# Kernel optimization log

Measured on AMD Instinct MI355X. Metric: run time of the kernel, lower is better.

## Reference

```python
import jax, jax.numpy as jnp
import numpy as np

INF = 10000000000.0
D_KEY = 1024


def setup_inputs() -> dict:
    key = jax.random.key(0)
    k1, k2, k3 = jax.random.split(key, 3)
    B, S, D = 8, 2048, D_KEY
    return {
        "query": jax.random.normal(k1, (B, S, D), dtype=jnp.float32),
        "key": jax.random.normal(k2, (B, S, D), dtype=jnp.float32),
        "value": jax.random.normal(k3, (B, S, D), dtype=jnp.float32),
    }


def reference(query, key, value):
    # dot_products: [B, S, S]
    scale = jnp.asarray(np.sqrt(D_KEY), dtype=query.dtype)
    dots = jnp.einsum("bqd,bkd->bqk", query, key)
    S = key.shape[1]
    # causal mask: subtract INF on strictly-upper-triangular entries
    # (original subtracts mask BEFORE dividing by scale)
    tri = jnp.triu(jnp.ones((S, S), dtype=dots.dtype), k=1) * INF
    dots = dots - tri[None, :, :]
    attn = jax.nn.softmax(dots / scale, axis=-1)
    return jnp.einsum("bqk,bkd->bqd", attn, value)
```

## Files before the change

kernel.cpp:

```cpp
#include <hip/hip_runtime.h>

#define BB 8
#define SS 2048
#define DD 1024

typedef float f32x4 __attribute__((ext_vector_type(4)));
typedef short s16x8 __attribute__((ext_vector_type(8)));
typedef short s16x4 __attribute__((ext_vector_type(4)));

__device__ __forceinline__ short f2bf(float f) {
  unsigned u = __float_as_uint(f);
  u += 0x7FFFu + ((u >> 16) & 1u);
  return (short)(u >> 16);
}

__global__ __launch_bounds__(256)
void cvt_bf16(const float* __restrict__ s0, const float* __restrict__ s1,
              short* __restrict__ d0, short* __restrict__ d1) {
  const float* s = (blockIdx.y == 0) ? s0 : s1;
  short*       d = (blockIdx.y == 0) ? d0 : d1;
  size_t i = ((size_t)blockIdx.x * 256 + threadIdx.x) * 4;
  float4 v = *(const float4*)(s + i);
  s16x4 h = { f2bf(v.x), f2bf(v.y), f2bf(v.z), f2bf(v.w) };
  *(s16x4*)(d + i) = h;
}

__global__ __launch_bounds__(256)
void cvt_vT(const float* __restrict__ V, short* __restrict__ Vt) {
  __shared__ float tile[64][65];
  const int b  = blockIdx.z;
  const int k0 = blockIdx.x * 64;
  const int d0 = blockIdx.y * 64;

  const float* src = V + ((size_t)b * SS + k0) * DD + d0;
  {
    int row = threadIdx.x >> 4;
    int col = (threadIdx.x & 15) * 4;
    #pragma unroll
    for (int i = 0; i < 4; ++i) {
      float4 v = *(const float4*)(src + (size_t)(row + i * 16) * DD + col);
      tile[row + i * 16][col + 0] = v.x;
      tile[row + i * 16][col + 1] = v.y;
      tile[row + i * 16][col + 2] = v.z;
      tile[row + i * 16][col + 3] = v.w;
    }
  }
  __syncthreads();
  {
    int d  = threadIdx.x & 63;
    int kc = (threadIdx.x >> 6) * 16;
    short* dst = Vt + ((size_t)b * DD + d0 + d) * SS + k0 + kc;
    s16x8 h0, h1;
    #pragma unroll
    for (int j = 0; j < 8; ++j) h0[j] = f2bf(tile[kc + j][d]);
    #pragma unroll
    for (int j = 0; j < 8; ++j) h1[j] = f2bf(tile[kc + 8 + j][d]);
    *(s16x8*)dst       = h0;
    *(s16x8*)(dst + 8) = h1;
  }
}

__global__ __launch_bounds__(512, 2)
void attn_fwd2(const short* __restrict__ Qb16, const short* __restrict__ Kb16,
               const short* __restrict__ Vtb16, float* __restrict__ Og) {
  int idx = blockIdx.x;
  int b, qt;
  if (idx < 256) { b = idx & 7; qt = 63 - (idx >> 3); }
  else           { int r = idx - 256; b = r & 7; qt = r >> 3; }
  const int q0  = qt * 32;
  const int nkt = qt / 2 + 1;

  const int tid  = threadIdx.x;
  const int lane = tid & 63;
  const int wave = tid >> 6;
  const int n15  = lane & 15;
  const int quad = lane >> 4;
  const int mh   = wave >> 2;
  const int nq   = wave & 3;

  __shared__ __align__(16) short qs[32][1032];
  __shared__ __align__(16) short ps[2][32][72];
  __shared__ float lred[4][32];

  const short* Qrow   = Qb16 + ((size_t)(b * SS + q0)) * DD;
  const short* Kbase  = Kb16 + ((size_t)b * SS) * DD;
  const short* Vtbase = Vtb16 + (size_t)b * DD * SS;

  {
    int row = tid >> 4;
    int c0  = (tid & 15) * 8;
    const short* src = Qrow + (size_t)row * DD;
    #pragma unroll
    for (int i = 0; i < 8; ++i)
      *(s16x8*)&qs[row][c0 + i * 128] = *(const s16x8*)(src + c0 + i * 128);
  }

  f32x4 acc[2][8];
  #pragma unroll
  for (int mt = 0; mt < 2; ++mt)
    #pragma unroll
    for (int nt = 0; nt < 8; ++nt)
      #pragma unroll
      for (int r = 0; r < 4; ++r) acc[mt][nt][r] = 0.0f;
  float lsum[4] = {0.f, 0.f, 0.f, 0.f};

  const short* Kln = Kbase + (size_t)(nq * 16 + n15) * DD + quad * 8;
  const short* Aln = &qs[mh * 16 + n15][quad * 8];
  const int dw = wave * 128;
  const short* Vln = Vtbase + (size_t)(dw + n15) * SS + quad * 8;

  __syncthreads();

  for (int kt = 0; kt < nkt; ++kt) {
    const int k0  = kt * 64;
    const int buf = kt & 1;

    const short* Kp = Kln + (size_t)k0 * DD;

    s16x8 kr[2][4];
    #pragma unroll
    for (int kk = 0; kk < 4; ++kk) kr[0][kk] = *(const s16x8*)(Kp + kk * 32);
    #pragma unroll
    for (int kk = 0; kk < 4; ++kk) kr[1][kk] = *(const s16x8*)(Kp + 128 + kk * 32);

    s16x8 bv0[8], bv1[8];
    {
      const short* Vp = Vln + k0;
      #pragma unroll
      for (int nt = 0; nt < 8; ++nt) {
        bv0[nt] = *(const s16x8*)(Vp + (size_t)(nt * 16) * SS);
        bv1[nt] = *(const s16x8*)(Vp + (size_t)(nt * 16) * SS + 32);
      }
    }

    f32x4 sfrag = {0.f, 0.f, 0.f, 0.f};
    #pragma unroll
    for (int dc = 0; dc < 8; ++dc) {
      #pragma unroll
      for (int kk = 0; kk < 4; ++kk) {
        s16x8 a = *(const s16x8*)(Aln + dc * 128 + kk * 32);
        sfrag = __builtin_amdgcn_mfma_f32_16x16x32_bf16(a, kr[dc & 1][kk], sfrag, 0, 0, 0);
      }
      if (dc < 6) {
        #pragma unroll
        for (int kk = 0; kk < 4; ++kk)
          kr[dc & 1][kk] = *(const s16x8*)(Kp + (dc + 2) * 128 + kk * 32);
      }
    }

    const int kcol = k0 + nq * 16 + n15;
    #pragma unroll
    for (int r = 0; r < 4; ++r) {
      int qrow = q0 + mh * 16 + quad * 4 + r;
      float sv = sfrag[r] * 0.03125f - 16.0f;
      float p  = (kcol > qrow) ? 0.0f : __expf(sv);
      lsum[r] += p;
      ps[buf][mh * 16 + quad * 4 + r][nq * 16 + n15] = f2bf(p);
    }

    __syncthreads();

    s16x8 a0 = *(const s16x8*)&ps[buf][n15][quad * 8];
    s16x8 a1 = *(const s16x8*)&ps[buf][16 + n15][quad * 8];
    #pragma unroll
    for (int nt = 0; nt < 8; ++nt) {
      acc[0][nt] = __builtin_amdgcn_mfma_f32_16x16x32_bf16(a0, bv0[nt], acc[0][nt], 0, 0, 0);
      acc[1][nt] = __builtin_amdgcn_mfma_f32_16x16x32_bf16(a1, bv0[nt], acc[1][nt], 0, 0, 0);
    }
    s16x8 a2 = *(const s16x8*)&ps[buf][n15][32 + quad * 8];
    s16x8 a3 = *(const s16x8*)&ps[buf][16 + n15][32 + quad * 8];
    #pragma unroll
    for (int nt = 0; nt < 8; ++nt) {
      acc[0][nt] = __builtin_amdgcn_mfma_f32_16x16x32_bf16(a2, bv1[nt], acc[0][nt], 0, 0, 0);
      acc[1][nt] = __builtin_amdgcn_mfma_f32_16x16x32_bf16(a3, bv1[nt], acc[1][nt], 0, 0, 0);
    }
  }

  #pragma unroll
  for (int off = 8; off >= 1; off >>= 1)
    #pragma unroll
    for (int r = 0; r < 4; ++r) lsum[r] += __shfl_xor(lsum[r], off);
  if (n15 == 0) {
    #pragma unroll
    for (int r = 0; r < 4; ++r) lred[nq][mh * 16 + quad * 4 + r] = lsum[r];
  }
  __syncthreads();
  float inv[2][4];
  #pragma unroll
  for (int mt = 0; mt < 2; ++mt)
    #pragma unroll
    for (int r = 0; r < 4; ++r) {
      int row = mt * 16 + quad * 4 + r;
      inv[mt][r] = 1.0f / (lred[0][row] + lred[1][row] + lred[2][row] + lred[3][row]);
    }
  float* Ob = Og + ((size_t)(b * SS + q0)) * DD + dw;
  #pragma unroll
  for (int mt = 0; mt < 2; ++mt)
    #pragma unroll
    for (int nt = 0; nt < 8; ++nt)
      #pragma unroll
      for (int r = 0; r < 4; ++r)
        Ob[(size_t)(mt * 16 + quad * 4 + r) * DD + nt * 16 + n15] =
            acc[mt][nt][r] * inv[mt][r];
}

__global__ __launch_bounds__(512, 2)
void attn_fwd(const float* __restrict__ Qg, const float* __restrict__ Kg,
              const float* __restrict__ Vg, float* __restrict__ Og) {
  int idx = blockIdx.x;
  int b, qt;
  if (idx < 256) { b = idx & 7; qt = 63 - (idx >> 3); }
  else           { int r = idx - 256; b = r & 7; qt = r >> 3; }
  const int q0  = qt * 32;
  const int nkt = (q0 + 31) / 64 + 1;

  const int tid  = threadIdx.x;
  const int lane = tid & 63;
  const int wave = tid >> 6;
  const int n15  = lane & 15;
  const int quad = lane >> 4;
  const int mh   = wave >> 2;
  const int nq   = wave & 3;

  __shared__ __align__(16) short qs[32][136];
  __shared__ __align__(16) short ks[64][136];
  __shared__ __align__(16) short vsT[1024][12];
  __shared__ __align__(16) short ps[32][72];
  __shared__ __align__(16) float red[32][4];
  __shared__ __align__(16) float mstate[32];
  __shared__ __align__(16) float lstate[32];
  __shared__ __align__(16) float alpha_s[32];

  const float* Qb = Qg + ((size_t)(b * SS + q0)) * DD;
  const float* Kb = Kg + ((size_t)(b * SS)) * DD;
  const float* Vb = Vg + ((size_t)(b * SS)) * DD;

  if (tid < 32) { mstate[tid] = -1e30f; lstate[tid] = 0.0f; }

  f32x4 acc[2][8];
  #pragma unroll
  for (int mt = 0; mt < 2; ++mt)
    #pragma unroll
    for (int nt = 0; nt < 8; ++nt)
      #pragma unroll
      for (int r = 0; r < 4; ++r) acc[mt][nt][r] = 0.0f;

  for (int kt = 0; kt < nkt; ++kt) {
    const int k0 = kt * 64;
    f32x4 sfrag;
    #pragma unroll
    for (int r = 0; r < 4; ++r) sfrag[r] = 0.0f;

    for (int dc = 0; dc < 8; ++dc) {
      __syncthreads();
      {
        int row = tid >> 4, c0 = tid & 15;
        const float4* src = (const float4*)(Qb + (size_t)row * DD + dc * 128);
        #pragma unroll
        for (int k2 = 0; k2 < 2; ++k2) {
          int c = c0 + 16 * k2;
          float4 v = src[c];
          s16x4 h = { f2bf(v.x), f2bf(v.y), f2bf(v.z), f2bf(v.w) };
          *(s16x4*)&qs[row][c * 4] = h;
        }
      }
      {
        int row = tid >> 3, c0 = tid & 7;
        const float4* src = (const float4*)(Kb + (size_t)(k0 + row) * DD + dc * 128);
        #pragma unroll
        for (int k2 = 0; k2 < 4; ++k2) {
          int c = c0 + 8 * k2;
          float4 v = src[c];
          s16x4 h = { f2bf(v.x), f2bf(v.y), f2bf(v.z), f2bf(v.w) };
          *(s16x4*)&ks[row][c * 4] = h;
        }
      }
      __syncthreads();
      #pragma unroll
      for (int kk = 0; kk < 4; ++kk) {
        s16x8 a  = *(const s16x8*)&qs[mh * 16 + n15][kk * 32 + quad * 8];
        s16x8 bb = *(const s16x8*)&ks[nq * 16 + n15][kk * 32 + quad * 8];
        sfrag = __builtin_amdgcn_mfma_f32_16x16x32_bf16(a, bb, sfrag, 0, 0, 0);
      }
    }

    float s[4], rmax[4];
    const int kcol = k0 + nq * 16 + n15;
    #pragma unroll
    for (int r = 0; r < 4; ++r) {
      int qrow = q0 + mh * 16 + quad * 4 + r;
      float v = sfrag[r] * 0.03125f;
      s[r] = (kcol > qrow) ? -1e30f : v;
      rmax[r] = s[r];
    }
    #pragma unroll
    for (int off = 8; off >= 1; off >>= 1)
      #pragma unroll
      for (int r = 0; r < 4; ++r)
        rmax[r] = fmaxf(rmax[r], __shfl_xor(rmax[r], off));
    if (n15 == 0) {
      #pragma unroll
      for (int r = 0; r < 4; ++r) red[mh * 16 + quad * 4 + r][nq] = rmax[r];
    }
    __syncthreads();
    if (tid < 32) {
      float mprev = mstate[tid];
      float tmax  = fmaxf(fmaxf(red[tid][0], red[tid][1]), fmaxf(red[tid][2], red[tid][3]));
      float mnew  = fmaxf(mprev, tmax);
      alpha_s[tid] = __expf(mprev - mnew);
      mstate[tid]  = mnew;
    }
    __syncthreads();
    {
      const float4 mr = *(const float4*)&mstate[mh * 16 + quad * 4];
      float p[4], psum[4];
      p[0] = __expf(s[0] - mr.x); p[1] = __expf(s[1] - mr.y);
      p[2] = __expf(s[2] - mr.z); p[3] = __expf(s[3] - mr.w);
      #pragma unroll
      for (int r = 0; r < 4; ++r) psum[r] = p[r];
      #pragma unroll
      for (int off = 8; off >= 1; off >>= 1)
        #pragma unroll
        for (int r = 0; r < 4; ++r) psum[r] += __shfl_xor(psum[r], off);
      if (n15 == 0) {
        #pragma unroll
        for (int r = 0; r < 4; ++r) red[mh * 16 + quad * 4 + r][nq] = psum[r];
      }
      #pragma unroll
      for (int r = 0; r < 4; ++r)
        ps[mh * 16 + quad * 4 + r][nq * 16 + n15] = f2bf(p[r]);
    }
    __syncthreads();
    if (tid < 32)
      lstate[tid] = lstate[tid] * alpha_s[tid]
                  + (red[tid][0] + red[tid][1] + red[tid][2] + red[tid][3]);

    {
      const float4 a0 = *(const float4*)&alpha_s[quad * 4];
      const float4 a1 = *(const float4*)&alpha_s[16 + quad * 4];
      #pragma unroll
      for (int nt = 0; nt < 8; ++nt) {
        acc[0][nt][0] *= a0.x; acc[0][nt][1] *= a0.y; acc[0][nt][2] *= a0.z; acc[0][nt][3] *= a0.w;
        acc[1][nt][0] *= a1.x; acc[1][nt][1] *= a1.y; acc[1][nt][2] *= a1.z; acc[1][nt][3] *= a1.w;
      }
    }

    #pragma unroll
    for (int kk2 = 0; kk2 < 2; ++kk2) {
      s16x8 bv[8];
      for (int h = 0; h < 4; ++h) {
        __syncthreads();
        {
          int j = tid & 7, c4b = tid >> 3;
          const float* src = Vb + (size_t)(k0 + kk2 * 32 + h * 8 + j) * DD;
          #pragma unroll
          for (int k4 = 0; k4 < 4; ++k4) {
            int c4 = c4b + 64 * k4;
            float4 v = ((const float4*)src)[c4];
            vsT[c4 * 4 + 0][j] = f2bf(v.x);
            vsT[c4 * 4 + 1][j] = f2bf(v.y);
            vsT[c4 * 4 + 2][j] = f2bf(v.z);
            vsT[c4 * 4 + 3][j] = f2bf(v.w);
          }
        }
        __syncthreads();
        if (quad == h) {
          #pragma unroll
          for (int nt = 0; nt < 8; ++nt) {
            int d = wave * 128 + nt * 16 + n15;
            s16x4 x0 = *(const s16x4*)&vsT[d][0];
            s16x4 x1 = *(const s16x4*)&vsT[d][4];
            bv[nt] = __builtin_shufflevector(x0, x1, 0, 1, 2, 3, 4, 5, 6, 7);
          }
        }
      }
      s16x8 a0 = *(const s16x8*)&ps[n15][kk2 * 32 + quad * 8];
      s16x8 a1 = *(const s16x8*)&ps[16 + n15][kk2 * 32 + quad * 8];
      #pragma unroll
      for (int nt = 0; nt < 8; ++nt) {
        acc[0][nt] = __builtin_amdgcn_mfma_f32_16x16x32_bf16(a0, bv[nt], acc[0][nt], 0, 0, 0);
        acc[1][nt] = __builtin_amdgcn_mfma_f32_16x16x32_bf16(a1, bv[nt], acc[1][nt], 0, 0, 0);
      }
    }
  }

  __syncthreads();
  {
    const float4 l0 = *(const float4*)&lstate[quad * 4];
    const float4 l1 = *(const float4*)&lstate[16 + quad * 4];
    float li0[4] = { 1.f / l0.x, 1.f / l0.y, 1.f / l0.z, 1.f / l0.w };
    float li1[4] = { 1.f / l1.x, 1.f / l1.y, 1.f / l1.z, 1.f / l1.w };
    float* Ob = Og + ((size_t)(b * SS + q0)) * DD;
    #pragma unroll
    for (int mt = 0; mt < 2; ++mt)
      #pragma unroll
      for (int nt = 0; nt < 8; ++nt)
        #pragma unroll
        for (int r = 0; r < 4; ++r) {
          int m = mt * 16 + quad * 4 + r;
          int d = wave * 128 + nt * 16 + n15;
          Ob[(size_t)m * DD + d] = acc[mt][nt][r] * (mt ? li1[r] : li0[r]);
        }
  }
}

extern "C" void kernel_launch(void* const* d_in, const int* in_sizes, int n_in,
                              void* d_out, int out_size, void* d_ws, size_t ws_size,
                              hipStream_t stream) {
  const float* Q = (const float*)d_in[0];
  const float* K = (const float*)d_in[1];
  const float* V = (const float*)d_in[2];
  float* O = (float*)d_out;
  (void)in_sizes; (void)n_in; (void)out_size;

  const size_t NE = (size_t)BB * SS * DD;
  if (ws_size >= 3 * NE * sizeof(short)) {
    short* Qb = (short*)d_ws;
    short* Kb = Qb + NE;
    short* Vt = Kb + NE;
    cvt_bf16<<<dim3((unsigned)(NE / 1024), 2), 256, 0, stream>>>(Q, K, Qb, Kb);
    cvt_vT<<<dim3(SS / 64, DD / 64, BB), 256, 0, stream>>>(V, Vt);
    attn_fwd2<<<dim3(512), dim3(512), 0, stream>>>(Qb, Kb, Vt, O);
  } else {
    attn_fwd<<<dim3(512), dim3(512), 0, stream>>>(Q, K, V, O);
  }
}
```

Before: 675.6 us.

## Use 64-row query tiles with split-K work balancing and atomic accumulation

The attention kernel now handles 64 query rows per block instead of 32, doubling reuse of each loaded K and V tile. For the long causal rows in the upper half, the key range is split across two blocks. Each block atomically adds its unnormalised partial output and row sums into a zeroed output and a workspace array, and a separate normalisation kernel divides at the end. This trades extra memsets, float atomics and one more pass over the output for better load balance and fewer global loads. The V transpose store mapping is also changed so a group of lanes writes contiguous segments of one row.

```diff
diff --git a/kernel.cpp b/kernel.cpp
--- a/kernel.cpp
+++ b/kernel.cpp
@@ -47,28 +47,41 @@
   }
   __syncthreads();
   {
-    int d  = threadIdx.x & 63;
-    int kc = (threadIdx.x >> 6) * 16;
-    short* dst = Vt + ((size_t)b * DD + d0 + d) * SS + k0 + kc;
+    int l  = threadIdx.x & 3;
+    int d  = threadIdx.x >> 2;
+    short* dst = Vt + ((size_t)b * DD + d0 + d) * SS + k0 + l * 16;
     s16x8 h0, h1;
     #pragma unroll
-    for (int j = 0; j < 8; ++j) h0[j] = f2bf(tile[kc + j][d]);
-    #pragma unroll
-    for (int j = 0; j < 8; ++j) h1[j] = f2bf(tile[kc + 8 + j][d]);
+    for (int j = 0; j < 8; ++j) h0[j] = f2bf(tile[l * 16 + j][d]);
+    #pragma unroll
+    for (int j = 0; j < 8; ++j) h1[j] = f2bf(tile[l * 16 + 8 + j][d]);
     *(s16x8*)dst       = h0;
     *(s16x8*)(dst + 8) = h1;
   }
 }
 
+template<int MODE>
 __global__ __launch_bounds__(512, 2)
-void attn_fwd2(const short* __restrict__ Qb16, const short* __restrict__ Kb16,
-               const short* __restrict__ Vtb16, float* __restrict__ Og) {
-  int idx = blockIdx.x;
-  int b, qt;
-  if (idx < 256) { b = idx & 7; qt = 63 - (idx >> 3); }
-  else           { int r = idx - 256; b = r & 7; qt = r >> 3; }
-  const int q0  = qt * 32;
-  const int nkt = qt / 2 + 1;
+void attn_fwd3(const short* __restrict__ Qb16, const short* __restrict__ Kb16,
+               const short* __restrict__ Vtb16, float* __restrict__ Og,
+               float* __restrict__ lg) {
+  const int idx = blockIdx.x;
+  const int b = idx & 7;
+  const int j = idx >> 3;
+  int qt, kt0, kt1;
+  if (MODE == 0) {
+    if (j < 32) {
+      qt = 16 + (j >> 1);
+      int h = (qt + 1) >> 1;
+      if (j & 1) { kt0 = h; kt1 = qt + 1; } else { kt0 = 0; kt1 = h; }
+    } else {
+      qt = j - 32; kt0 = 0; kt1 = qt + 1;
+    }
+  } else {
+    qt = j; kt0 = 0; kt1 = qt + 1;
+  }
+  const bool whole = (kt0 == 0) && (kt1 == qt + 1);
+  const int q0 = qt * 64;
 
   const int tid  = threadIdx.x;
   const int lane = tid & 63;
@@ -78,40 +91,41 @@
   const int mh   = wave >> 2;
   const int nq   = wave & 3;
 
-  __shared__ __align__(16) short qs[32][1032];
-  __shared__ __align__(16) short ps[2][32][72];
-  __shared__ float lred[4][32];
+  __shared__ __align__(16) short qs[64][1032];
+  __shared__ __align__(16) short ps[2][64][72];
+  __shared__ float lred[4][64];
 
   const short* Qrow   = Qb16 + ((size_t)(b * SS + q0)) * DD;
   const short* Kbase  = Kb16 + ((size_t)b * SS) * DD;
   const short* Vtbase = Vtb16 + (size_t)b * DD * SS;
 
   {
-    int row = tid >> 4;
-    int c0  = (tid & 15) * 8;
+    int row = tid >> 3;
+    int c0  = (tid & 7) * 8;
     const short* src = Qrow + (size_t)row * DD;
     #pragma unroll
-    for (int i = 0; i < 8; ++i)
-      *(s16x8*)&qs[row][c0 + i * 128] = *(const s16x8*)(src + c0 + i * 128);
-  }
-
-  f32x4 acc[2][8];
+    for (int i = 0; i < 16; ++i)
+      *(s16x8*)&qs[row][c0 + i * 64] = *(const s16x8*)(src + c0 + i * 64);
+  }
+
+  f32x4 acc[4][8];
   #pragma unroll
-  for (int mt = 0; mt < 2; ++mt)
+  for (int m = 0; m < 4; ++m)
     #pragma unroll
     for (int nt = 0; nt < 8; ++nt)
       #pragma unroll
-      for (int r = 0; r < 4; ++r) acc[mt][nt][r] = 0.0f;
-  float lsum[4] = {0.f, 0.f, 0.f, 0.f};
-
-  const short* Kln = Kbase + (size_t)(nq * 16 + n15) * DD + quad * 8;
-  const short* Aln = &qs[mh * 16 + n15][quad * 8];
+      for (int r = 0; r < 4; ++r) acc[m][nt][r] = 0.0f;
+  float lsum[2][4] = {{0.f,0.f,0.f,0.f},{0.f,0.f,0.f,0.f}};
+
+  const short* Kln  = Kbase + (size_t)(nq * 16 + n15) * DD + quad * 8;
+  const short* Aln0 = &qs[mh * 32 + n15][quad * 8];
+  const short* Aln1 = &qs[mh * 32 + 16 + n15][quad * 8];
   const int dw = wave * 128;
   const short* Vln = Vtbase + (size_t)(dw + n15) * SS + quad * 8;
 
   __syncthreads();
 
-  for (int kt = 0; kt < nkt; ++kt) {
+  for (int kt = kt0; kt < kt1; ++kt) {
     const int k0  = kt * 64;
     const int buf = kt & 1;
 
@@ -133,13 +147,15 @@
       }
     }
 
-    f32x4 sfrag = {0.f, 0.f, 0.f, 0.f};
+    f32x4 sfA = {0.f,0.f,0.f,0.f}, sfB = {0.f,0.f,0.f,0.f};
     #pragma unroll
     for (int dc = 0; dc < 8; ++dc) {
       #pragma unroll
       for (int kk = 0; kk < 4; ++kk) {
-        s16x8 a = *(const s16x8*)(Aln + dc * 128 + kk * 32);
-        sfrag = __builtin_amdgcn_mfma_f32_16x16x32_bf16(a, kr[dc & 1][kk], sfrag, 0, 0, 0);
+        s16x8 a0 = *(const s16x8*)(Aln0 + dc * 128 + kk * 32);
+        s16x8 a1 = *(const s16x8*)(Aln1 + dc * 128 + kk * 32);
+        sfA = __builtin_amdgcn_mfma_f32_16x16x32_bf16(a0, kr[dc & 1][kk], sfA, 0, 0, 0);
+        sfB = __builtin_amdgcn_mfma_f32_16x16x32_bf16(a1, kr[dc & 1][kk], sfB, 0, 0, 0);
       }
       if (dc < 6) {
         #pragma unroll
@@ -150,58 +166,106 @@
 
     const int kcol = k0 + nq * 16 + n15;
     #pragma unroll
-    for (int r = 0; r < 4; ++r) {
-      int qrow = q0 + mh * 16 + quad * 4 + r;
-      float sv = sfrag[r] * 0.03125f - 16.0f;
-      float p  = (kcol > qrow) ? 0.0f : __expf(sv);
-      lsum[r] += p;
-      ps[buf][mh * 16 + quad * 4 + r][nq * 16 + n15] = f2bf(p);
+    for (int t = 0; t < 2; ++t) {
+      const f32x4 sf = t ? sfB : sfA;
+      const int rowb = mh * 32 + t * 16 + quad * 4;
+      #pragma unroll
+      for (int r = 0; r < 4; ++r) {
+        int qrow = q0 + rowb + r;
+        float sv = sf[r] * 0.03125f - 16.0f;
+        float p  = (kcol > qrow) ? 0.0f : __expf(sv);
+        lsum[t][r] += p;
+        ps[buf][rowb + r][nq * 16 + n15] = f2bf(p);
+      }
     }
 
     __syncthreads();
 
-    s16x8 a0 = *(const s16x8*)&ps[buf][n15][quad * 8];
-    s16x8 a1 = *(const s16x8*)&ps[buf][16 + n15][quad * 8];
-    #pragma unroll
-    for (int nt = 0; nt < 8; ++nt) {
-      acc[0][nt] = __builtin_amdgcn_mfma_f32_16x16x32_bf16(a0, bv0[nt], acc[0][nt], 0, 0, 0);
-      acc[1][nt] = __builtin_amdgcn_mfma_f32_16x16x32_bf16(a1, bv0[nt], acc[1][nt], 0, 0, 0);
-    }
-    s16x8 a2 = *(const s16x8*)&ps[buf][n15][32 + quad * 8];
-    s16x8 a3 = *(const s16x8*)&ps[buf][16 + n15][32 + quad * 8];
-    #pragma unroll
-    for (int nt = 0; nt < 8; ++nt) {
-      acc[0][nt] = __builtin_amdgcn_mfma_f32_16x16x32_bf16(a2, bv1[nt], acc[0][nt], 0, 0, 0);
-      acc[1][nt] = __builtin_amdgcn_mfma_f32_16x16x32_bf16(a3, bv1[nt], acc[1][nt], 0, 0, 0);
+    #pragma unroll
+    for (int kk2 = 0; kk2 < 2; ++kk2) {
+      s16x8 a0 = *(const s16x8*)&ps[buf][ 0 + n15][kk2 * 32 + quad * 8];
+      s16x8 a1 = *(const s16x8*)&ps[buf][16 + n15][kk2 * 32 + quad * 8];
+      s16x8 a2 = *(const s16x8*)&ps[buf][32 + n15][kk2 * 32 + quad * 8];
+      s16x8 a3 = *(const s16x8*)&ps[buf][48 + n15][kk2 * 32 + quad * 8];
+      #pragma unroll
+      for (int nt = 0; nt < 8; ++nt) {
+        s16x8 bv = kk2 ? bv1[nt] : bv0[nt];
+        acc[0][nt] = __builtin_amdgcn_mfma_f32_16x16x32_bf16(a0, bv, acc[0][nt], 0, 0, 0);
+        acc[1][nt] = __builtin_amdgcn_mfma_f32_16x16x32_bf16(a1, bv, acc[1][nt], 0, 0, 0);
+        acc[2][nt] = __builtin_amdgcn_mfma_f32_16x16x32_bf16(a2, bv, acc[2][nt], 0, 0, 0);
+        acc[3][nt] = __builtin_amdgcn_mfma_f32_16x16x32_bf16(a3, bv, acc[3][nt], 0, 0, 0);
+      }
     }
   }
 
   #pragma unroll
   for (int off = 8; off >= 1; off >>= 1)
     #pragma unroll
-    for (int r = 0; r < 4; ++r) lsum[r] += __shfl_xor(lsum[r], off);
+    for (int t = 0; t < 2; ++t)
+      #pragma unroll
+      for (int r = 0; r < 4; ++r) lsum[t][r] += __shfl_xor(lsum[t][r], off);
   if (n15 == 0) {
     #pragma unroll
-    for (int r = 0; r < 4; ++r) lred[nq][mh * 16 + quad * 4 + r] = lsum[r];
+    for (int t = 0; t < 2; ++t)
+      #pragma unroll
+      for (int r = 0; r < 4; ++r)
+        lred[nq][mh * 32 + t * 16 + quad * 4 + r] = lsum[t][r];
   }
   __syncthreads();
-  float inv[2][4];
-  #pragma unroll
-  for (int mt = 0; mt < 2; ++mt)
-    #pragma unroll
-    for (int r = 0; r < 4; ++r) {
-      int row = mt * 16 + quad * 4 + r;
-      inv[mt][r] = 1.0f / (lred[0][row] + lred[1][row] + lred[2][row] + lred[3][row]);
-    }
+
   float* Ob = Og + ((size_t)(b * SS + q0)) * DD + dw;
-  #pragma unroll
-  for (int mt = 0; mt < 2; ++mt)
-    #pragma unroll
-    for (int nt = 0; nt < 8; ++nt)
-      #pragma unroll
-      for (int r = 0; r < 4; ++r)
-        Ob[(size_t)(mt * 16 + quad * 4 + r) * DD + nt * 16 + n15] =
-            acc[mt][nt][r] * inv[mt][r];
+
+  if (MODE == 0) {
+    if (tid < 64) {
+      float rs = lred[0][tid] + lred[1][tid] + lred[2][tid] + lred[3][tid];
+      atomicAdd(lg + (size_t)b * SS + q0 + tid, rs);
+    }
+    if (whole) {
+      #pragma unroll
+      for (int m = 0; m < 4; ++m)
+        #pragma unroll
+        for (int nt = 0; nt < 8; ++nt)
+          #pragma unroll
+          for (int r = 0; r < 4; ++r)
+            Ob[(size_t)(m * 16 + quad * 4 + r) * DD + nt * 16 + n15] = acc[m][nt][r];
+    } else {
+      #pragma unroll
+      for (int m = 0; m < 4; ++m)
+        #pragma unroll
+        for (int nt = 0; nt < 8; ++nt)
+          #pragma unroll
+          for (int r = 0; r < 4; ++r)
+            atomicAdd(&Ob[(size_t)(m * 16 + quad * 4 + r) * DD + nt * 16 + n15],
+                      acc[m][nt][r]);
+    }
+  } else {
+    float inv[4][4];
+    #pragma unroll
+    for (int m = 0; m < 4; ++m)
+      #pragma unroll
+      for (int r = 0; r < 4; ++r) {
+        int row = m * 16 + quad * 4 + r;
+        inv[m][r] = 1.0f / (lred[0][row] + lred[1][row] + lred[2][row] + lred[3][row]);
+      }
+    #pragma unroll
+    for (int m = 0; m < 4; ++m)
+      #pragma unroll
+      for (int nt = 0; nt < 8; ++nt)
+        #pragma unroll
+        for (int r = 0; r < 4; ++r)
+          Ob[(size_t)(m * 16 + quad * 4 + r) * DD + nt * 16 + n15] =
+              acc[m][nt][r] * inv[m][r];
+  }
+}
+
+__global__ __launch_bounds__(256)
+void norm_o(float* __restrict__ O, const float* __restrict__ lg) {
+  const int row = blockIdx.x;
+  const float inv = 1.0f / lg[row];
+  float4* p = (float4*)(O + (size_t)row * DD) + threadIdx.x;
+  float4 v = *p;
+  v.x *= inv; v.y *= inv; v.z *= inv; v.w *= inv;
+  *p = v;
 }
 
 __global__ __launch_bounds__(512, 2)
@@ -351,16 +415,16 @@
       for (int h = 0; h < 4; ++h) {
         __syncthreads();
         {
-          int j = tid & 7, c4b = tid >> 3;
-          const float* src = Vb + (size_t)(k0 + kk2 * 32 + h * 8 + j) * DD;
+          int jj = tid & 7, c4b = tid >> 3;
+          const float* src = Vb + (size_t)(k0 + kk2 * 32 + h * 8 + jj) * DD;
           #pragma unroll
           for (int k4 = 0; k4 < 4; ++k4) {
             int c4 = c4b + 64 * k4;
             float4 v = ((const float4*)src)[c4];
-            vsT[c4 * 4 + 0][j] = f2bf(v.x);
-            vsT[c4 * 4 + 1][j] = f2bf(v.y);
-            vsT[c4 * 4 + 2][j] = f2bf(v.z);
-            vsT[c4 * 4 + 3][j] = f2bf(v.w);
+            vsT[c4 * 4 + 0][jj] = f2bf(v.x);
+            vsT[c4 * 4 + 1][jj] = f2bf(v.y);
+            vsT[c4 * 4 + 2][jj] = f2bf(v.z);
+            vsT[c4 * 4 + 3][jj] = f2bf(v.w);
           }
         }
         __syncthreads();
@@ -411,16 +475,30 @@
   const float* K = (const float*)d_in[1];
   const float* V = (const float*)d_in[2];
   float* O = (float*)d_out;
-  (void)in_sizes; (void)n_in; (void)out_size;
-
-  const size_t NE = (size_t)BB * SS * DD;
-  if (ws_size >= 3 * NE * sizeof(short)) {
+  (void)in_sizes; (void)n_in;
+
+  const size_t NE      = (size_t)BB * SS * DD;
+  const size_t needQKV = 3 * NE * sizeof(short);
+  const size_t needL   = (size_t)BB * SS * sizeof(float);
+
+  if (ws_size >= needQKV + needL) {
+    short* Qb = (short*)d_ws;
+    short* Kb = Qb + NE;
+    short* Vt = Kb + NE;
+    float* lg = (float*)((char*)d_ws + needQKV);
+    hipMemsetAsync(d_out, 0, out_size, stream);
+    hipMemsetAsync(lg, 0, needL, stream);
+    cvt_bf16<<<dim3((unsigned)(NE / 1024), 2), 256, 0, stream>>>(Q, K, Qb, Kb);
+    cvt_vT<<<dim3(SS / 64, DD / 64, BB), 256, 0, stream>>>(V, Vt);
+    attn_fwd3<0><<<dim3(384), dim3(512), 0, stream>>>(Qb, Kb, Vt, O, lg);
+    norm_o<<<dim3(BB * SS), dim3(256), 0, stream>>>(O, lg);
+  } else if (ws_size >= needQKV) {
     short* Qb = (short*)d_ws;
     short* Kb = Qb + NE;
     short* Vt = Kb + NE;
     cvt_bf16<<<dim3((unsigned)(NE / 1024), 2), 256, 0, stream>>>(Q, K, Qb, Kb);
     cvt_vT<<<dim3(SS / 64, DD / 64, BB), 256, 0, stream>>>(V, Vt);
-    attn_fwd2<<<dim3(512), dim3(512), 0, stream>>>(Qb, Kb, Vt, O);
+    attn_fwd3<1><<<dim3(256), dim3(512), 0, stream>>>(Qb, Kb, Vt, O, nullptr);
   } else {
     attn_fwd<<<dim3(512), dim3(512), 0, stream>>>(Q, K, V, O);
   }
```

Result: faster. 577.8 us (-14.5%).
